# Kernel tuning notes

Measured on AMD Instinct MI355X. Metric: run time of the kernel, lower is better.

The kernel has to match this reference:

```python
import jax, jax.numpy as jnp
import numpy as np

IN_COUNT = 1024
OUT_COUNT = 1024
NUM_BASIS = 8
INPUT_ABS_MAX = 1.0
X_MIN = 0.0
X_MAX = 1.0
GAMMA_SCALE = 3.0
BATCH = 4096


def setup_inputs() -> dict:
    key = jax.random.key(0)
    k_x, k_c = jax.random.split(key)
    x = jax.random.normal(k_x, (BATCH, IN_COUNT), dtype=jnp.float32)
    coeffs = 0.01 * jax.random.normal(k_c, (OUT_COUNT, IN_COUNT, NUM_BASIS), dtype=jnp.float32)
    # fixed buffers
    centers_1d = jnp.linspace(X_MIN, X_MAX, NUM_BASIS)
    centers = jnp.broadcast_to(centers_1d[None, :], (IN_COUNT, NUM_BASIS)).astype(jnp.float32)
    delta = (X_MAX - X_MIN) / (NUM_BASIS - 1)
    gamma = GAMMA_SCALE / delta
    slopes = jnp.full((IN_COUNT, NUM_BASIS), gamma, dtype=jnp.float32)
    alpha = jnp.full((IN_COUNT,), (X_MAX - X_MIN) / (2.0 * INPUT_ABS_MAX), dtype=jnp.float32)
    beta = jnp.full((IN_COUNT,), 0.5 * (X_MIN + X_MAX), dtype=jnp.float32)
    return {"x": x, "coeffs": coeffs, "centers": centers, "slopes": slopes, "alpha": alpha, "beta": beta}


def reference(x, coeffs, centers, slopes, alpha, beta):
    # u: (B, in) affine transform with fixed alpha/beta
    u = alpha[None, :] * x + beta[None, :]
    # basis: (B, in, basis) = 0.5*(1+tanh(slope*(u - center)))
    basis = 0.5 * (1.0 + jnp.tanh(slopes[None, :, :] * (u[:, :, None] - centers[None, :, :])))
    # y[b,o] = sum_{i,m} coeffs[o,i,m] * basis[b,i,m]  (fused GEMM over in*basis)
    y = jnp.einsum('bim,oim->bo', basis, coeffs)
    return y
```

## Files before the change

kernel.cpp:

```cpp
#include <hip/hip_runtime.h>
#include <hip/hip_bf16.h>
#include <cstdint>
#include <cstddef>

#define BATCH 4096
#define INC   1024
#define OUTC  1024
#define NB    8
#define KDIM  (INC * NB)

#define BM 256
#define BN 128
#define BKB 64
#define SPLITS 4
#define KZ (KDIM / SPLITS)
#define KSTEPS (KZ / BKB)
#define GRID_BLOCKS ((OUTC / BN) * (BATCH / BM) * SPLITS)

#define EXPAND_BLOCKS  ((BATCH * INC) / 256)
#define QUANT_BLOCKS   OUTC
#define PREP_BLOCKS    (EXPAND_BLOCKS + QUANT_BLOCKS)

typedef int      v4i __attribute__((ext_vector_type(4)));
typedef unsigned v4u __attribute__((ext_vector_type(4)));
typedef char     v8c __attribute__((ext_vector_type(8)));

__device__ __forceinline__ unsigned short f2bf(float f) {
  union { float f; unsigned u; } v; v.f = f;
  unsigned r = v.u + 0x7fffu + ((v.u >> 16) & 1u);
  return (unsigned short)(r >> 16);
}
__device__ __forceinline__ float bf2f(unsigned short h) {
  union { unsigned u; float f; } v; v.u = ((unsigned)h) << 16; return v.f;
}

__device__ __forceinline__ void gld16(const char* g, char* l) {
  __builtin_amdgcn_global_load_lds(
      (const __attribute__((address_space(1))) unsigned int*)g,
      (__attribute__((address_space(3))) unsigned int*)l, 16, 0, 0);
}

__global__ __launch_bounds__(256) void prep_kernel(
    const float* __restrict__ x, const float4* __restrict__ coeffs4,
    const float* __restrict__ centers, const float* __restrict__ slopes,
    const float* __restrict__ alpha, const float* __restrict__ beta,
    char* __restrict__ Ai8, int* __restrict__ Ci8i,
    float* __restrict__ maxrow, int* __restrict__ qcsum) {
  const int blk = blockIdx.x;
  const int tid = threadIdx.x;
  if (blk < EXPAND_BLOCKS) {
    const int idx = blk * 256 + tid;
    const int i = idx & (INC - 1);
    const float u = alpha[i] * x[idx] + beta[i];
    const float s0 = slopes[i * NB];
    const float c0 = centers[i * NB];
    const float c1 = centers[i * NB + 1];
    const float L2E2 = 2.8853900817779268f;
    const float a2 = L2E2 * s0;
    float e = __builtin_amdgcn_exp2f(a2 * (c0 - u));
    const float R = __builtin_amdgcn_exp2f(a2 * (c1 - c0));
    v8c q;
#pragma unroll
    for (int m = 0; m < 8; ++m) {
      float basis = __builtin_amdgcn_rcpf(1.0f + e);
      q[m] = (char)(int)rintf(basis * 254.0f - 127.0f);
      e *= R;
    }
    *(v8c*)(Ai8 + (size_t)idx * 8) = q;
  } else {
    const int o = blk - EXPAND_BLOCKS;
    const float4* row = coeffs4 + (size_t)o * (KDIM / 4);
    float4 v[8];
    float m = 0.0f;
#pragma unroll
    for (int j = 0; j < 8; ++j) {
      v[j] = row[tid + 256 * j];
      m = fmaxf(m, fmaxf(fmaxf(fabsf(v[j].x), fabsf(v[j].y)),
                         fmaxf(fabsf(v[j].z), fabsf(v[j].w))));
    }
#pragma unroll
    for (int off = 32; off; off >>= 1) m = fmaxf(m, __shfl_xor(m, off));
    __shared__ float wm[4];
    __shared__ int   wq[4];
    if ((tid & 63) == 0) wm[tid >> 6] = m;
    __syncthreads();
    const float M = fmaxf(fmaxf(fmaxf(wm[0], wm[1]), fmaxf(wm[2], wm[3])), 1e-30f);
    const float s = 127.0f / M;
    int qs = 0;
#pragma unroll
    for (int j = 0; j < 8; ++j) {
      int q0 = (int)rintf(v[j].x * s), q1 = (int)rintf(v[j].y * s);
      int q2 = (int)rintf(v[j].z * s), q3 = (int)rintf(v[j].w * s);
      Ci8i[(size_t)o * (KDIM / 4) + tid + 256 * j] =
          (q0 & 0xFF) | ((q1 & 0xFF) << 8) | ((q2 & 0xFF) << 16) | ((q3 & 0xFF) << 24);
      qs += q0 + q1 + q2 + q3;
    }
#pragma unroll
    for (int off = 32; off; off >>= 1) qs += __shfl_xor(qs, off);
    if ((tid & 63) == 0) wq[tid >> 6] = qs;
    __syncthreads();
    if (tid == 0) { maxrow[o] = M; qcsum[o] = wq[0] + wq[1] + wq[2] + wq[3]; }
  }
}

__global__ __launch_bounds__(512, 4) void gemm_kernel(
    const char* __restrict__ A, const char* __restrict__ C,
    unsigned* __restrict__ partials) {
  __shared__ __align__(16) char As[2][BM * BKB];
  __shared__ __align__(16) char Bs[2][BN * BKB];

  const int id = (blockIdx.x & 7) * (GRID_BLOCKS / 8) + (blockIdx.x >> 3);
  const int z  = id >> 7;
  const int p  = id & 127;
  const int by = p >> 3;
  const int bx = p & 7;
  const int bm0 = by * BM;
  const int bn0 = bx * BN;
  const int kt0 = z * KZ;

  const int tid  = threadIdx.x;
  const int wave = tid >> 6;
  const int lane = tid & 63;
  const int quad = lane >> 4;
  const int lm   = lane & 15;
  const int wm   = (wave >> 1) * 64;
  const int wn   = (wave & 1) * 64;

  const int r4 = lane >> 2;
  const int gg = (lane & 3) ^ ((lane >> 3) & 3);

  const char* pA0 = A + (size_t)(bm0 + wave * 32 + r4) * KDIM + kt0 + gg * 16;
  const char* pB0 = C + (size_t)(bn0 + wave * 16 + r4) * KDIM + kt0 + gg * 16;
  const int loA = wave * 32 * BKB;
  const int loB = wave * 16 * BKB;

  v4i acc[4][4] = {};
  const int kx = (quad ^ ((lm >> 1) & 3)) * 16;

#define STAGE(SL)                                                            \
  {                                                                          \
    gld16(pA0,                      As[SL] + loA);                           \
    gld16(pA0 + (size_t)16 * KDIM,  As[SL] + loA + 16 * BKB);                \
    gld16(pB0,                      Bs[SL] + loB);                           \
    pA0 += BKB; pB0 += BKB;                                                  \
  }

  STAGE(0);
  STAGE(1);

  for (int t = 0; t < KSTEPS; ++t) {
    const int cur = t & 1;
    if (t < KSTEPS - 1) {
      asm volatile("s_waitcnt vmcnt(3)" ::: "memory");
    } else {
      asm volatile("s_waitcnt vmcnt(0)" ::: "memory");
    }
    __builtin_amdgcn_sched_barrier(0);
    __builtin_amdgcn_s_barrier();

    const char* cA = As[cur];
    const char* cB = Bs[cur];
    v4i a[4], b[4];
#pragma unroll
    for (int f = 0; f < 4; ++f)
      a[f] = *(const v4i*)(cA + (wm + f * 16 + lm) * BKB + kx);
#pragma unroll
    for (int f = 0; f < 4; ++f)
      b[f] = *(const v4i*)(cB + (wn + f * 16 + lm) * BKB + kx);

    __builtin_amdgcn_s_setprio(1);
#pragma unroll
    for (int fm = 0; fm < 4; ++fm)
#pragma unroll
      for (int fn = 0; fn < 4; ++fn)
        acc[fm][fn] = __builtin_amdgcn_mfma_i32_16x16x64_i8(a[fm], b[fn], acc[fm][fn], 0, 0, 0);
    __builtin_amdgcn_s_setprio(0);

    __builtin_amdgcn_s_barrier();
    if (t < KSTEPS - 2) STAGE(cur);
  }
#undef STAGE

  unsigned w32[32];
#pragma unroll
  for (int fm = 0; fm < 4; ++fm)
#pragma unroll
    for (int fn = 0; fn < 4; ++fn)
#pragma unroll
      for (int rr = 0; rr < 2; ++rr)
        w32[fm * 8 + fn * 2 + rr] =
            (unsigned)f2bf((float)acc[fm][fn][2 * rr]) |
            ((unsigned)f2bf((float)acc[fm][fn][2 * rr + 1]) << 16);

  unsigned* outp = partials + (((size_t)z * 128 + p) * 8 + wave) * 2048 + lane * 4;
#pragma unroll
  for (int c = 0; c < 8; ++c)
    *(v4u*)(outp + c * 256) = v4u{w32[4 * c], w32[4 * c + 1], w32[4 * c + 2], w32[4 * c + 3]};
}

__global__ __launch_bounds__(256) void reduce_kernel(
    const unsigned* __restrict__ P, const float* __restrict__ maxrow,
    const int* __restrict__ qcsum, float* __restrict__ out) {
  const int blk = blockIdx.x;
  const int p = blk >> 3, w = blk & 7;
  const int bm0 = (p >> 3) * BM, bn0 = (p & 7) * BN;
  const int B0 = bm0 + (w >> 1) * 64;
  const int O0 = bn0 + (w & 1) * 64;
  const int t = threadIdx.x;

  __shared__ float tile[64][65];
  __shared__ float sM[64];
  __shared__ float sQ[64];
  if (t < 64) { sM[t] = maxrow[O0 + t]; sQ[t] = 127.0f * (float)qcsum[O0 + t]; }
  __syncthreads();

  const size_t base = ((size_t)p * 8 + w) * 2048 + (size_t)t * 8;
  const size_t zs   = (size_t)128 * 8 * 2048;
  float slo[8] = {}, shi[8] = {};
#pragma unroll
  for (int z = 0; z < SPLITS; ++z) {
    v4u ua = *(const v4u*)(P + z * zs + base);
    v4u ub = *(const v4u*)(P + z * zs + base + 4);
#pragma unroll
    for (int k = 0; k < 4; ++k) {
      slo[k]     += bf2f((unsigned short)(ua[k] & 0xFFFFu));
      shi[k]     += bf2f((unsigned short)(ua[k] >> 16));
      slo[k + 4] += bf2f((unsigned short)(ub[k] & 0xFFFFu));
      shi[k + 4] += bf2f((unsigned short)(ub[k] >> 16));
    }
  }
  const float inv = 1.0f / 32258.0f;
#pragma unroll
  for (int k = 0; k < 8; ++k) {
    const int W  = t * 8 + k;
    const int c  = W >> 8;
    const int l  = (W >> 2) & 63;
    const int j  = (c << 2) | (W & 3);
    const int fm = j >> 3, fn = (j >> 1) & 3, rr = j & 1;
    const int bl = fm * 16 + (l >> 4) * 4 + rr * 2;
    const int ol = fn * 16 + (l & 15);
    const float M = sM[ol], corr = sQ[ol];
    tile[bl][ol]     = M * (slo[k] + corr) * inv;
    tile[bl + 1][ol] = M * (shi[k] + corr) * inv;
  }
  __syncthreads();

  const int row = t >> 2;
  const int c0  = (t & 3) * 16;
  float* op = out + (size_t)(B0 + row) * OUTC + O0 + c0;
#pragma unroll
  for (int i = 0; i < 4; ++i) {
    *(float4*)(op + 4 * i) = float4{tile[row][c0 + 4 * i],     tile[row][c0 + 4 * i + 1],
                                    tile[row][c0 + 4 * i + 2], tile[row][c0 + 4 * i + 3]};
  }
}

extern "C" void kernel_launch(void* const* d_in, const int* in_sizes, int n_in,
                              void* d_out, int out_size, void* d_ws, size_t ws_size,
                              hipStream_t stream) {
  const float* x       = (const float*)d_in[0];
  const float* coeffs  = (const float*)d_in[1];
  const float* centers = (const float*)d_in[2];
  const float* slopes  = (const float*)d_in[3];
  const float* alpha   = (const float*)d_in[4];
  const float* beta    = (const float*)d_in[5];
  float* out = (float*)d_out;

  const size_t a_bytes    = (size_t)BATCH * KDIM;
  const size_t c_bytes    = (size_t)OUTC * KDIM;
  const size_t stat_bytes = OUTC * sizeof(float);
  const size_t qcs_bytes  = OUTC * sizeof(int);
  const size_t part_bytes = (size_t)SPLITS * BATCH * OUTC * 2;
  if (ws_size < a_bytes + c_bytes + stat_bytes + qcs_bytes + part_bytes) return;

  char*  Ai8    = (char*)d_ws;
  char*  Ci8    = Ai8 + a_bytes;
  float* maxrow = (float*)(Ci8 + c_bytes);
  int*   qcsum  = (int*)((char*)maxrow + stat_bytes);
  unsigned* parts = (unsigned*)((char*)qcsum + qcs_bytes);

  prep_kernel<<<PREP_BLOCKS, 256, 0, stream>>>(
      x, (const float4*)coeffs, centers, slopes, alpha, beta,
      Ai8, (int*)Ci8, maxrow, qcsum);

  gemm_kernel<<<GRID_BLOCKS, 512, 0, stream>>>(Ai8, Ci8, parts);

  reduce_kernel<<<128 * 8, 256, 0, stream>>>(parts, maxrow, qcsum, out);
}
```

Before: 155.6 us.

## Enlarge GEMM tile to 256x256 with register-staged global loads

Doubles the block tile in N so each wave computes a 128x64 output, raising reuse of LDS fragments per MFMA. Replaces direct global-to-LDS loads with register-staged double buffering, where global loads are issued ahead and written to the alternate LDS buffer during the compute step. Adjusts the partials layout and the reduce kernel to match the larger tile. This halves the grid to 256 blocks and lowers occupancy to 2 blocks per CU, with more register pressure from 32 accumulators and staging registers.

```diff
diff --git a/kernel.cpp b/kernel.cpp
--- a/kernel.cpp
+++ b/kernel.cpp
@@ -10,12 +10,13 @@
 #define KDIM  (INC * NB)
 
 #define BM 256
-#define BN 128
+#define BN 256
 #define BKB 64
 #define SPLITS 4
 #define KZ (KDIM / SPLITS)
 #define KSTEPS (KZ / BKB)
 #define GRID_BLOCKS ((OUTC / BN) * (BATCH / BM) * SPLITS)
+#define FRAG (16 * BKB)
 
 #define EXPAND_BLOCKS  ((BATCH * INC) / 256)
 #define QUANT_BLOCKS   OUTC
@@ -32,12 +33,6 @@
 }
 __device__ __forceinline__ float bf2f(unsigned short h) {
   union { unsigned u; float f; } v; v.u = ((unsigned)h) << 16; return v.f;
-}
-
-__device__ __forceinline__ void gld16(const char* g, char* l) {
-  __builtin_amdgcn_global_load_lds(
-      (const __attribute__((address_space(1))) unsigned int*)g,
-      (__attribute__((address_space(3))) unsigned int*)l, 16, 0, 0);
 }
 
 __global__ __launch_bounds__(256) void prep_kernel(
@@ -103,17 +98,17 @@
   }
 }
 
-__global__ __launch_bounds__(512, 4) void gemm_kernel(
+__global__ __launch_bounds__(512, 2) void gemm_kernel(
     const char* __restrict__ A, const char* __restrict__ C,
     unsigned* __restrict__ partials) {
   __shared__ __align__(16) char As[2][BM * BKB];
   __shared__ __align__(16) char Bs[2][BN * BKB];
 
   const int id = (blockIdx.x & 7) * (GRID_BLOCKS / 8) + (blockIdx.x >> 3);
-  const int z  = id >> 7;
-  const int p  = id & 127;
-  const int by = p >> 3;
-  const int bx = p & 7;
+  const int z  = id >> 6;
+  const int p  = id & 63;
+  const int by = p >> 2;
+  const int bx = p & 3;
   const int bm0 = by * BM;
   const int bn0 = bx * BN;
   const int kt0 = z * KZ;
@@ -123,67 +118,87 @@
   const int lane = tid & 63;
   const int quad = lane >> 4;
   const int lm   = lane & 15;
-  const int wm   = (wave >> 1) * 64;
-  const int wn   = (wave & 1) * 64;
+  const int wm   = (wave >> 2) * 128;
+  const int wn   = (wave & 3) * 64;
 
   const int r4 = lane >> 2;
   const int gg = (lane & 3) ^ ((lane >> 3) & 3);
 
   const char* pA0 = A + (size_t)(bm0 + wave * 32 + r4) * KDIM + kt0 + gg * 16;
-  const char* pB0 = C + (size_t)(bn0 + wave * 16 + r4) * KDIM + kt0 + gg * 16;
-  const int loA = wave * 32 * BKB;
-  const int loB = wave * 16 * BKB;
-
-  v4i acc[4][4] = {};
-  const int kx = (quad ^ ((lm >> 1) & 3)) * 16;
-
-#define STAGE(SL)                                                            \
+  const char* pB0 = C + (size_t)(bn0 + wave * 32 + r4) * KDIM + kt0 + gg * 16;
+  const int lo = wave * 32 * BKB;
+
+  const int kx   = (quad ^ ((lm >> 1) & 3)) * 16;
+  const int aoff = (wm + lm) * BKB + kx;
+  const int boff = (wn + lm) * BKB + kx;
+
+  v4i acc[8][4] = {};
+  v4u g0A0, g0A1, g0B0, g0B1;
+  v4u g1A0, g1A1, g1B0, g1B1;
+
+#define GLOAD(A0, A1, B0, B1)                                                \
   {                                                                          \
-    gld16(pA0,                      As[SL] + loA);                           \
-    gld16(pA0 + (size_t)16 * KDIM,  As[SL] + loA + 16 * BKB);                \
-    gld16(pB0,                      Bs[SL] + loB);                           \
+    A0 = *(const v4u*)(pA0);                                                 \
+    A1 = *(const v4u*)(pA0 + (size_t)16 * KDIM);                             \
+    B0 = *(const v4u*)(pB0);                                                 \
+    B1 = *(const v4u*)(pB0 + (size_t)16 * KDIM);                             \
     pA0 += BKB; pB0 += BKB;                                                  \
   }
 
-  STAGE(0);
-  STAGE(1);
-
-  for (int t = 0; t < KSTEPS; ++t) {
-    const int cur = t & 1;
-    if (t < KSTEPS - 1) {
-      asm volatile("s_waitcnt vmcnt(3)" ::: "memory");
-    } else {
-      asm volatile("s_waitcnt vmcnt(0)" ::: "memory");
-    }
-    __builtin_amdgcn_sched_barrier(0);
-    __builtin_amdgcn_s_barrier();
-
-    const char* cA = As[cur];
-    const char* cB = Bs[cur];
-    v4i a[4], b[4];
-#pragma unroll
-    for (int f = 0; f < 4; ++f)
-      a[f] = *(const v4i*)(cA + (wm + f * 16 + lm) * BKB + kx);
-#pragma unroll
-    for (int f = 0; f < 4; ++f)
-      b[f] = *(const v4i*)(cB + (wn + f * 16 + lm) * BKB + kx);
-
-    __builtin_amdgcn_s_setprio(1);
-#pragma unroll
-    for (int fm = 0; fm < 4; ++fm)
-#pragma unroll
-      for (int fn = 0; fn < 4; ++fn)
-        acc[fm][fn] = __builtin_amdgcn_mfma_i32_16x16x64_i8(a[fm], b[fn], acc[fm][fn], 0, 0, 0);
-    __builtin_amdgcn_s_setprio(0);
-
-    __builtin_amdgcn_s_barrier();
-    if (t < KSTEPS - 2) STAGE(cur);
-  }
-#undef STAGE
-
-  unsigned w32[32];
-#pragma unroll
-  for (int fm = 0; fm < 4; ++fm)
+#define DSWRITE(SL, A0, A1, B0, B1)                                          \
+  {                                                                          \
+    *(v4u*)(As[SL] + lo + lane * 16)            = A0;                        \
+    *(v4u*)(As[SL] + lo + 16 * BKB + lane * 16) = A1;                        \
+    *(v4u*)(Bs[SL] + lo + lane * 16)            = B0;                        \
+    *(v4u*)(Bs[SL] + lo + 16 * BKB + lane * 16) = B1;                        \
+  }
+
+#define GSTEP(CUR, LA0, LA1, LB0, LB1, WA0, WA1, WB0, WB1, DOGLOAD, DOWRITE, DOBAR) \
+  {                                                                          \
+    if (DOGLOAD) GLOAD(LA0, LA1, LB0, LB1)                                   \
+    const char* cA = As[CUR] + aoff;                                         \
+    const char* cB = Bs[CUR] + boff;                                         \
+    v4i a[8], b[4];                                                          \
+    _Pragma("unroll")                                                        \
+    for (int f = 0; f < 4; ++f) a[f] = *(const v4i*)(cA + f * FRAG);         \
+    _Pragma("unroll")                                                        \
+    for (int f = 0; f < 4; ++f) b[f] = *(const v4i*)(cB + f * FRAG);         \
+    _Pragma("unroll")                                                        \
+    for (int f = 4; f < 8; ++f) a[f] = *(const v4i*)(cA + f * FRAG);         \
+    if (DOWRITE) DSWRITE(CUR ^ 1, WA0, WA1, WB0, WB1)                        \
+    __builtin_amdgcn_s_setprio(1);                                           \
+    _Pragma("unroll")                                                        \
+    for (int fm = 0; fm < 4; ++fm)                                           \
+      _Pragma("unroll")                                                      \
+      for (int fn = 0; fn < 4; ++fn)                                         \
+        acc[fm][fn] = __builtin_amdgcn_mfma_i32_16x16x64_i8(a[fm], b[fn], acc[fm][fn], 0, 0, 0); \
+    _Pragma("unroll")                                                        \
+    for (int fm = 4; fm < 8; ++fm)                                           \
+      _Pragma("unroll")                                                      \
+      for (int fn = 0; fn < 4; ++fn)                                         \
+        acc[fm][fn] = __builtin_amdgcn_mfma_i32_16x16x64_i8(a[fm], b[fn], acc[fm][fn], 0, 0, 0); \
+    __builtin_amdgcn_s_setprio(0);                                           \
+    if (DOBAR) __syncthreads();                                              \
+  }
+
+  GLOAD(g0A0, g0A1, g0B0, g0B1)
+  GLOAD(g1A0, g1A1, g1B0, g1B1)
+  DSWRITE(0, g0A0, g0A1, g0B0, g0B1)
+  __syncthreads();
+
+  for (int i = 0; i < 15; ++i) {
+    GSTEP(0, g0A0, g0A1, g0B0, g0B1, g1A0, g1A1, g1B0, g1B1, true, true, true)
+    GSTEP(1, g1A0, g1A1, g1B0, g1B1, g0A0, g0A1, g0B0, g0B1, true, true, true)
+  }
+  GSTEP(0, g0A0, g0A1, g0B0, g0B1, g1A0, g1A1, g1B0, g1B1, false, true, true)
+  GSTEP(1, g1A0, g1A1, g1B0, g1B1, g0A0, g0A1, g0B0, g0B1, false, false, false)
+#undef GSTEP
+#undef DSWRITE
+#undef GLOAD
+
+  unsigned w32[64];
+#pragma unroll
+  for (int fm = 0; fm < 8; ++fm)
 #pragma unroll
     for (int fn = 0; fn < 4; ++fn)
 #pragma unroll
@@ -192,9 +207,9 @@
             (unsigned)f2bf((float)acc[fm][fn][2 * rr]) |
             ((unsigned)f2bf((float)acc[fm][fn][2 * rr + 1]) << 16);
 
-  unsigned* outp = partials + (((size_t)z * 128 + p) * 8 + wave) * 2048 + lane * 4;
-#pragma unroll
-  for (int c = 0; c < 8; ++c)
+  unsigned* outp = partials + (((size_t)z * 64 + p) * 8 + wave) * 4096 + lane * 4;
+#pragma unroll
+  for (int c = 0; c < 16; ++c)
     *(v4u*)(outp + c * 256) = v4u{w32[4 * c], w32[4 * c + 1], w32[4 * c + 2], w32[4 * c + 3]};
 }
 
@@ -203,56 +218,55 @@
     const int* __restrict__ qcsum, float* __restrict__ out) {
   const int blk = blockIdx.x;
   const int p = blk >> 3, w = blk & 7;
-  const int bm0 = (p >> 3) * BM, bn0 = (p & 7) * BN;
-  const int B0 = bm0 + (w >> 1) * 64;
-  const int O0 = bn0 + (w & 1) * 64;
+  const int by = p >> 2, bx = p & 3;
+  const int B0 = by * BM + (w >> 2) * 128;
+  const int O0 = bx * BN + (w & 3) * 64;
   const int t = threadIdx.x;
-
-  __shared__ float tile[64][65];
+  const int l = t & 63;
+
+  __shared__ float tile[128][65];
   __shared__ float sM[64];
   __shared__ float sQ[64];
   if (t < 64) { sM[t] = maxrow[O0 + t]; sQ[t] = 127.0f * (float)qcsum[O0 + t]; }
   __syncthreads();
 
-  const size_t base = ((size_t)p * 8 + w) * 2048 + (size_t)t * 8;
-  const size_t zs   = (size_t)128 * 8 * 2048;
-  float slo[8] = {}, shi[8] = {};
+  const size_t region = ((size_t)p * 8 + w) * 4096;
+  const size_t zs     = (size_t)64 * 8 * 4096;
+  float slo[16] = {}, shi[16] = {};
 #pragma unroll
   for (int z = 0; z < SPLITS; ++z) {
-    v4u ua = *(const v4u*)(P + z * zs + base);
-    v4u ub = *(const v4u*)(P + z * zs + base + 4);
-#pragma unroll
-    for (int k = 0; k < 4; ++k) {
-      slo[k]     += bf2f((unsigned short)(ua[k] & 0xFFFFu));
-      shi[k]     += bf2f((unsigned short)(ua[k] >> 16));
-      slo[k + 4] += bf2f((unsigned short)(ub[k] & 0xFFFFu));
-      shi[k + 4] += bf2f((unsigned short)(ub[k] >> 16));
+#pragma unroll
+    for (int r = 0; r < 4; ++r) {
+      v4u u = *(const v4u*)(P + z * zs + region + ((t >> 6) + r * 4) * 256 + l * 4);
+#pragma unroll
+      for (int i = 0; i < 4; ++i) {
+        slo[r * 4 + i] += bf2f((unsigned short)(u[i] & 0xFFFFu));
+        shi[r * 4 + i] += bf2f((unsigned short)(u[i] >> 16));
+      }
     }
   }
   const float inv = 1.0f / 32258.0f;
 #pragma unroll
-  for (int k = 0; k < 8; ++k) {
-    const int W  = t * 8 + k;
-    const int c  = W >> 8;
-    const int l  = (W >> 2) & 63;
-    const int j  = (c << 2) | (W & 3);
-    const int fm = j >> 3, fn = (j >> 1) & 3, rr = j & 1;
-    const int bl = fm * 16 + (l >> 4) * 4 + rr * 2;
-    const int ol = fn * 16 + (l & 15);
-    const float M = sM[ol], corr = sQ[ol];
-    tile[bl][ol]     = M * (slo[k] + corr) * inv;
-    tile[bl + 1][ol] = M * (shi[k] + corr) * inv;
-  }
+  for (int r = 0; r < 4; ++r)
+#pragma unroll
+    for (int i = 0; i < 4; ++i) {
+      const int jj = (t >> 6) * 4 + r * 16 + i;
+      const int fm = jj >> 3, fn = (jj >> 1) & 3, rr = jj & 1;
+      const int bl = fm * 16 + (l >> 4) * 4 + rr * 2;
+      const int ol = fn * 16 + (l & 15);
+      const float M = sM[ol], corr = sQ[ol];
+      tile[bl][ol]     = M * (slo[r * 4 + i] + corr) * inv;
+      tile[bl + 1][ol] = M * (shi[r * 4 + i] + corr) * inv;
+    }
   __syncthreads();
 
-  const int row = t >> 2;
-  const int c0  = (t & 3) * 16;
+  const int row = t >> 1;
+  const int c0  = (t & 1) * 32;
   float* op = out + (size_t)(B0 + row) * OUTC + O0 + c0;
 #pragma unroll
-  for (int i = 0; i < 4; ++i) {
+  for (int i = 0; i < 8; ++i)
     *(float4*)(op + 4 * i) = float4{tile[row][c0 + 4 * i],     tile[row][c0 + 4 * i + 1],
                                     tile[row][c0 + 4 * i + 2], tile[row][c0 + 4 * i + 3]};
-  }
 }
 
 extern "C" void kernel_launch(void* const* d_in, const int* in_sizes, int n_in,
@@ -285,5 +299,5 @@
 
   gemm_kernel<<<GRID_BLOCKS, 512, 0, stream>>>(Ai8, Ci8, parts);
 
-  reduce_kernel<<<128 * 8, 256, 0, stream>>>(parts, maxrow, qcsum, out);
-}
+  reduce_kernel<<<64 * 8, 256, 0, stream>>>(parts, maxrow, qcsum, out);
+}
```

New measurement: 152.6 us. Within noise of the previous version (-1.9%).
